# Performance work log

Hardware: AMD Instinct MI355X
Metric: run time of the kernel (lower is better)

## Reference

```python
import jax, jax.numpy as jnp
import numpy as np
from jax import lax

B, H, W = 2, 256, 256
K = 7
K2 = K * K
IN_CH = 32 * 2 + 81  # 145


def _conv(x, w, b):
    y = lax.conv_general_dilated(x, w, (1, 1), 'SAME', dimension_numbers=('NCHW', 'OIHW', 'NCHW'))
    return y + b[None, :, None, None]


def _lrelu(x):
    return jnp.where(x >= 0, x, 0.1 * x)


def _predictor(x, w1, b1, w2, b2, w3, b3, wo, bo, ww, bw):
    f = _lrelu(_conv(x, w1, b1))
    f = _lrelu(_conv(f, w2, b2))
    f = _lrelu(_conv(f, w3, b3))
    offsets = _conv(f, wo, bo)                     # (B, 2*K2, H, W)
    weights = jax.nn.softmax(_conv(f, ww, bw), 1)  # (B, K2, H, W)
    return offsets, weights


def _sample(image, offsets, weights):
    b, c, h, w = image.shape
    k2 = weights.shape[1]
    off = offsets.reshape(b, k2, 2, h, w)
    dx, dy = off[:, :, 0], off[:, :, 1]
    gy, gx = jnp.meshgrid(jnp.arange(h, dtype=image.dtype), jnp.arange(w, dtype=image.dtype), indexing='ij')
    sx = gx[None, None] + dx  # (b,k2,h,w)
    sy = gy[None, None] + dy
    # Original normalizes with 2*s/(n-1)-1 (align_corners=True formula) but calls
    # grid_sample(align_corners=False): pixel coord = ((g+1)*n - 1)/2 = s*n/(n-1) - 0.5.
    # padding_mode='border' == clamp coord to [0, n-1] before bilinear.
    px = jnp.clip(sx * (w / (w - 1.0)) - 0.5, 0.0, w - 1.0)
    py = jnp.clip(sy * (h / (h - 1.0)) - 0.5, 0.0, h - 1.0)
    x0 = jnp.floor(px)
    y0 = jnp.floor(py)
    fx = (px - x0)[:, None]  # (b,1,k2,h,w)
    fy = (py - y0)[:, None]
    x0i = x0.astype(jnp.int32)
    y0i = y0.astype(jnp.int32)
    x1i = jnp.minimum(x0i + 1, w - 1)
    y1i = jnp.minimum(y0i + 1, h - 1)
    img = image.reshape(b, c, h * w)

    def gather(yi, xi):
        idx = (yi * w + xi).reshape(b, 1, k2 * h * w)
        return jnp.take_along_axis(img, idx, axis=2).reshape(b, c, k2, h, w)

    v00 = gather(y0i, x0i)
    v01 = gather(y0i, x1i)
    v10 = gather(y1i, x0i)
    v11 = gather(y1i, x1i)
    sampled = (v00 * (1 - fx) * (1 - fy) + v01 * fx * (1 - fy)
               + v10 * (1 - fx) * fy + v11 * fx * fy)
    return jnp.einsum('bkhw,bckhw->bchw', weights, sampled)


def setup_inputs() -> dict:
    key = jax.random.key(0)
    ks = iter(jax.random.split(key, 64))

    def nrm(shape, s=1.0):
        return jax.random.normal(next(ks), shape, jnp.float32) * s

    off0 = np.array([[j - K // 2, i - K // 2] for i in range(K) for j in range(K)],
                    np.float32).reshape(-1)  # interleaved (dx, dy) default grid

    def pred_params(p):
        return {
            p + '_w1': nrm((256, IN_CH, 3, 3), 0.02), p + '_b1': jnp.zeros((256,), jnp.float32),
            p + '_w2': nrm((256, 256, 3, 3), 0.02), p + '_b2': jnp.zeros((256,), jnp.float32),
            p + '_w3': nrm((128, 256, 3, 3), 0.02), p + '_b3': jnp.zeros((128,), jnp.float32),
            p + '_wo': nrm((2 * K2, 128, 3, 3), 0.01), p + '_bo': jnp.asarray(off0),
            p + '_ww': nrm((K2, 128, 3, 3), 0.02), p + '_bw': jnp.full((K2,), 1.0 / K2, jnp.float32),
        }

    inp = {
        'frame1': nrm((B, 3, H, W)),
        'frame2': nrm((B, 3, H, W)),
        'feat1': nrm((B, 32, H, W)),
        'feat2': nrm((B, 32, H, W)),
        'corr': nrm((B, 81, H, W)),
    }
    inp.update(pred_params('k1'))
    inp.update(pred_params('k2'))
    inp['bl_w1'] = nrm((64, IN_CH, 3, 3), 0.02)
    inp['bl_b1'] = jnp.zeros((64,), jnp.float32)
    inp['bl_w2'] = nrm((1, 64, 3, 3), 0.02)
    inp['bl_b2'] = jnp.zeros((1,), jnp.float32)
    return inp


def reference(frame1, frame2, feat1, feat2, corr,
              k1_w1, k1_b1, k1_w2, k1_b2, k1_w3, k1_b3, k1_wo, k1_bo, k1_ww, k1_bw,
              k2_w1, k2_b1, k2_w2, k2_b2, k2_w3, k2_b3, k2_wo, k2_bo, k2_ww, k2_bw,
              bl_w1, bl_b1, bl_w2, bl_b2):
    combined = jnp.concatenate([feat1, feat2, corr], axis=1)  # (B,145,H,W)
    off1, wt1 = _predictor(combined, k1_w1, k1_b1, k1_w2, k1_b2, k1_w3, k1_b3, k1_wo, k1_bo, k1_ww, k1_bw)
    off2, wt2 = _predictor(combined, k2_w1, k2_b1, k2_w2, k2_b2, k2_w3, k2_b3, k2_wo, k2_bo, k2_ww, k2_bw)
    s1 = _sample(frame1, off1, wt1)
    s2 = _sample(frame2, off2, wt2)
    blend = jax.nn.sigmoid(_conv(_lrelu(_conv(combined, bl_w1, bl_b1)), bl_w2, bl_b2))
    output = blend * s1 + (1.0 - blend) * s2
    return (output, blend, off1, off2, wt1, wt2)
```

## Files before the change

### kernel.cpp

```cpp
#include <hip/hip_runtime.h>


static constexpr int HW  = 65536;
static constexpr int WID = 256;
static constexpr int PAD = 66564;

using f32x4  = __attribute__((ext_vector_type(4))) float;
using s16x8  = __attribute__((ext_vector_type(8))) short;

__device__ __forceinline__ unsigned short f2b(float f) {
    unsigned u = __builtin_bit_cast(unsigned, f);
    u += 0x7fffu + ((u >> 16) & 1u);
    return (unsigned short)(u >> 16);
}
__device__ __forceinline__ float b2f(unsigned short h) {
    unsigned u = ((unsigned)h) << 16;
    return __builtin_bit_cast(float, u);
}

template <int N> __device__ __forceinline__ void vm_wait() {
    asm volatile("s_waitcnt vmcnt(%0)" :: "n"(N) : "memory");
}

__global__ void pack_x(const float* __restrict__ feat1, const float* __restrict__ feat2,
                       const float* __restrict__ corr, unsigned short* __restrict__ Xc) {
    int idx = blockIdx.x * 256 + threadIdx.x;
    int g  = idx >> 17;
    int bp = idx & (2 * HW - 1);
    int b  = bp >> 16, p = bp & 65535;
    unsigned short v[8];
#pragma unroll
    for (int j = 0; j < 8; ++j) {
        int c = g * 8 + j;
        float val = 0.f;
        if (c < 32)       val = feat1[(size_t)(b * 32 + c) * HW + p];
        else if (c < 64)  val = feat2[(size_t)(b * 32 + (c - 32)) * HW + p];
        else if (c < 145) val = corr [(size_t)(b * 81 + (c - 64)) * HW + p];
        v[j] = f2b(val);
    }
    uint4 u;
    u.x = v[0] | ((unsigned)v[1] << 16);
    u.y = v[2] | ((unsigned)v[3] << 16);
    u.z = v[4] | ((unsigned)v[5] << 16);
    u.w = v[6] | ((unsigned)v[7] << 16);
    int y = p >> 8, x = p & 255;
    size_t cell = (size_t)b * PAD + (size_t)(y + 1) * 258 + (x + 1);
    *reinterpret_cast<uint4*>(Xc + cell * 160 + g * 8) = u;
}

__global__ void pack_w(const float* __restrict__ W, unsigned short* __restrict__ Wp,
                       int OC, int IC, int OCP, int KC) {
    int idx = blockIdx.x * 256 + threadIdx.x;
    int total = 9 * KC * 4 * OCP * 8;
    if (idx >= total) return;
    int i8 = idx & 7;  int r = idx >> 3;
    int oc = r % OCP;  r /= OCP;
    int g  = r & 3;    r >>= 2;
    int kb = r % KC;   int s = r / KC;
    int ic = kb * 32 + g * 8 + i8;
    float v = (oc < OC && ic < IC) ? W[((size_t)(oc * IC + ic)) * 9 + s] : 0.f;
    Wp[idx] = f2b(v);
}

__global__ void zero_border(unsigned short* __restrict__ buf, int C) {
    int idx = blockIdx.x * 256 + threadIdx.x;
    int G = C >> 3;
    int total = 2 * 1028 * G;
    if (idx >= total) return;
    int gi = idx % G; int r = idx / G;
    int ci = r % 1028; int b = r / 1028;
    int row, col;
    if (ci < 258)      { row = 0;            col = ci; }
    else if (ci < 516) { row = 257;          col = ci - 258; }
    else if (ci < 772) { row = ci - 516 + 1; col = 0; }
    else               { row = ci - 772 + 1; col = 257; }
    *reinterpret_cast<uint4*>(buf + ((size_t)b * PAD + row * 258 + col) * C + gi * 8) =
        make_uint4(0u, 0u, 0u, 0u);
}

template <int ICP, int OCF, int OCT, int MODE>
__global__ __launch_bounds__(512, 2) void conv3x3(
    const unsigned short* __restrict__ X,
    const uint4* __restrict__ Wp,
    const float* __restrict__ bias,
    unsigned short* __restrict__ outB,
    float* __restrict__ outF)
{
    constexpr int KC  = ICP / 32;
    constexpr int MF  = OCF / 32;
    constexpr int WST = OCF / 128;
    constexpr int WGR = OCF * 4;
    __shared__ uint4 lds[3072 + 3 * WGR];

    const int t = threadIdx.x;
    const int lane = t & 63;
    const int wv = t >> 6;
    const int wm = wv >> 2, wn = wv & 3;
    const int l15 = lane & 15, kq = lane >> 4;

    const int bid = blockIdx.x;
    const int work = ((bid & 7) << 6) | (bid >> 3);
    const int bb = work >> 8;
    const int tt = work & 255;
    const int tr = tt >> 3, tc = tt & 7;

    unsigned xoff[3];
#pragma unroll
    for (int it = 0; it < 3; ++it) {
        int G = it * 512 + t;
        int g = G / 384;
        int cell = G - g * 384;
        cell = min(cell, 339);
        int rr = cell / 34, cc = cell - rr * 34;
        xoff[it] = (unsigned)(((bb * PAD + (tr * 8 + rr) * 258 + tc * 32 + cc) * ICP
                               + g * 8) * 2);
    }
    const int tdst = t & ~63;

    auto gload = [&](const char* src, uint4* dst) {
        __builtin_amdgcn_global_load_lds(
            (const __attribute__((address_space(1))) unsigned int*)src,
            (__attribute__((address_space(3))) unsigned int*)dst, 16, 0, 0);
    };
    auto stage_x = [&](int slot) {
#pragma unroll
        for (int it = 0; it < 3; ++it)
            gload((const char*)X + xoff[it], &lds[slot * 1536 + it * 512 + tdst]);
    };
    auto stage_w = [&](int s2, int kb2, int slot) {
        const unsigned base = (unsigned)(s2 * KC + kb2) * (unsigned)(WGR * 16);
#pragma unroll
        for (int it = 0; it < WST; ++it)
            gload((const char*)Wp + base + (unsigned)((it * 512 + t) * 16),
                  &lds[3072 + slot * WGR + it * 512 + tdst]);
    };

    const unsigned aLane = (unsigned)((kq * OCF + wm * (OCF / 2) + l15) * 16) + 49152u;
    const unsigned bLane = (unsigned)((kq * 384 + wn * 68 + l15) * 16);
    const char* ldsc = (const char*)lds;

    f32x4 acc[MF][4] = {};

    stage_x(0);
    stage_w(0, 0, 0);
    stage_w(1, 0, 1);
    vm_wait<WST>();
    __builtin_amdgcn_s_barrier();

#pragma unroll 1
    for (int kb = 0; kb < KC; ++kb) {
        const unsigned bBase = bLane + (unsigned)((kb & 1) * 24576);
#pragma unroll
        for (int s = 0; s < 9; ++s) {
            const int dy = s / 3, dx = s - 3 * (s / 3);
            const unsigned aBase = aLane + (unsigned)((s % 3) * (WGR * 16));

            uint4 aR[MF], bR[4];
#pragma unroll
            for (int fm = 0; fm < MF; ++fm)
                aR[fm] = *(const uint4*)(ldsc + aBase + (unsigned)(fm * 256));
#pragma unroll
            for (int fn = 0; fn < 4; ++fn)
                bR[fn] = *(const uint4*)(ldsc + bBase +
                    (unsigned)(((((fn >> 1) + dy) * 34) + (fn & 1) * 16 + dx) * 16));

            if (s < 7) {
                stage_w(s + 2, kb, (s + 2) % 3);
            } else if (kb + 1 < KC) {
                stage_w(s - 7, kb + 1, (s + 2) % 3);
            }
            if (s == 0 && kb + 1 < KC) {
#pragma unroll
                for (int it = 0; it < 3; ++it) xoff[it] += 64u;
                stage_x((kb + 1) & 1);
            }

            __builtin_amdgcn_s_barrier();
            asm volatile("s_waitcnt lgkmcnt(0)" ::: "memory");
            __builtin_amdgcn_sched_barrier(0);
            __builtin_amdgcn_s_setprio(1);
#pragma unroll
            for (int fm = 0; fm < MF; ++fm)
#pragma unroll
                for (int fn = 0; fn < 4; ++fn)
                    acc[fm][fn] = __builtin_amdgcn_mfma_f32_16x16x32_bf16(
                        __builtin_bit_cast(s16x8, aR[fm]),
                        __builtin_bit_cast(s16x8, bR[fn]),
                        acc[fm][fn], 0, 0, 0);
            __builtin_amdgcn_s_setprio(0);

            if (s == 0) {
                if (kb + 1 < KC) vm_wait<WST + 3>(); else vm_wait<WST>();
            } else if (s < 7) {
                vm_wait<WST>();
            } else {
                if (kb + 1 < KC) vm_wait<WST>(); else vm_wait<0>();
            }
            __builtin_amdgcn_s_barrier();
        }
    }

#pragma unroll
    for (int fm = 0; fm < MF; ++fm) {
#pragma unroll
        for (int fn = 0; fn < 4; ++fn) {
            const int prow = wn * 2 + (fn >> 1);
            const int pcol = (fn & 1) * 16 + l15;
            const int oc0 = wm * (OCF / 2) + fm * 16 + kq * 4;
            if (MODE == 0) {
                if (oc0 < OCT) {
                    const size_t cellp = (size_t)bb * PAD +
                        (size_t)(tr * 8 + prow + 1) * 258 + tc * 32 + pcol + 1;
                    float4 bv = *reinterpret_cast<const float4*>(bias + oc0);
                    const float* bvp = reinterpret_cast<const float*>(&bv);
                    unsigned short o[4];
#pragma unroll
                    for (int j = 0; j < 4; ++j) {
                        float r = acc[fm][fn][j] + bvp[j];
                        r = (r >= 0.f) ? r : 0.1f * r;
                        o[j] = f2b(r);
                    }
                    uint2 pk;
                    pk.x = o[0] | ((unsigned)o[1] << 16);
                    pk.y = o[2] | ((unsigned)o[3] << 16);
                    *reinterpret_cast<uint2*>(outB + cellp * OCT + oc0) = pk;
                }
            } else {
                const int py = tr * 8 + prow, px = tc * 32 + pcol;
#pragma unroll
                for (int j = 0; j < 4; ++j) {
                    const int oc = oc0 + j;
                    if (oc < OCT)
                        outF[((size_t)bb * OCT + oc) * HW + py * WID + px] =
                            acc[fm][fn][j] + bias[oc];
                }
            }
        }
    }
}

__global__ void softmax49(float* __restrict__ L) {
    int idx = blockIdx.x * 256 + threadIdx.x;
    int b = idx >> 16, p = idx & 65535;
    float* lp = L + (size_t)b * 49 * HW + p;
    float v[49];
    float mx = -1e30f;
#pragma unroll
    for (int k = 0; k < 49; ++k) { v[k] = lp[(size_t)k * HW]; mx = fmaxf(mx, v[k]); }
    float sum = 0.f;
#pragma unroll
    for (int k = 0; k < 49; ++k) { v[k] = expf(v[k] - mx); sum += v[k]; }
    float inv = 1.f / sum;
#pragma unroll
    for (int k = 0; k < 49; ++k) lp[(size_t)k * HW] = v[k] * inv;
}

__global__ void blend2k(const unsigned short* __restrict__ Fb, const float* __restrict__ W2,
                        const float* __restrict__ B2, float* __restrict__ blendOut) {
    int idx = blockIdx.x * 256 + threadIdx.x;
    int b = idx >> 16, p = idx & 65535, y = p >> 8, x = p & 255;
    float acc = B2[0];
#pragma unroll
    for (int ry = 0; ry < 3; ++ry) {
#pragma unroll
        for (int rx = 0; rx < 3; ++rx) {
            const unsigned short* fp = Fb + ((size_t)b * PAD + (size_t)(y + ry) * 258 + (x + rx)) * 64;
#pragma unroll
            for (int g = 0; g < 8; ++g) {
                uint4 u = *reinterpret_cast<const uint4*>(fp + g * 8);
                unsigned w[4] = {u.x, u.y, u.z, u.w};
#pragma unroll
                for (int h = 0; h < 4; ++h) {
                    int c = g * 8 + h * 2;
                    acc += b2f((unsigned short)(w[h] & 0xffffu)) * W2[(c)     * 9 + ry * 3 + rx];
                    acc += b2f((unsigned short)(w[h] >> 16))     * W2[(c + 1) * 9 + ry * 3 + rx];
                }
            }
        }
    }
    blendOut[idx] = 1.f / (1.f + expf(-acc));
}

__global__ void pack_frames(const float* __restrict__ f1, const float* __restrict__ f2,
                            f32x4* __restrict__ Ff) {
    int idx = blockIdx.x * 256 + threadIdx.x;
    int fr = idx >> 17; int bp = idx & (2 * HW - 1);
    const float* src = fr ? f2 : f1;
    int b = bp >> 16, p = bp & 65535;
    f32x4 v;
    v[0] = src[(size_t)(b * 3 + 0) * HW + p];
    v[1] = src[(size_t)(b * 3 + 1) * HW + p];
    v[2] = src[(size_t)(b * 3 + 2) * HW + p];
    v[3] = 0.f;
    Ff[(size_t)fr * 2 * HW + bp] = v;
}

__device__ __forceinline__ void sample_accum4(const f32x4* __restrict__ img,
                                              const float* __restrict__ off,
                                              const float* __restrict__ wt,
                                              int x, int y, f32x4& s) {
    for (int k = 0; k < 49; ++k) {
        float dx = off[(size_t)(2 * k) * HW];
        float dy = off[(size_t)(2 * k + 1) * HW];
        float w  = wt [(size_t)k * HW];
        float px = ((float)x + dx) * (256.f / 255.f) - 0.5f;
        float py = ((float)y + dy) * (256.f / 255.f) - 0.5f;
        px = fminf(fmaxf(px, 0.f), 255.f);
        py = fminf(fmaxf(py, 0.f), 255.f);
        float x0f = floorf(px), y0f = floorf(py);
        float fx = px - x0f, fy = py - y0f;
        int x0 = (int)x0f, y0 = (int)y0f;
        int x1 = min(x0 + 1, 255), y1 = min(y0 + 1, 255);
        const f32x4* r0 = img + y0 * WID;
        const f32x4* r1 = img + y1 * WID;
        f32x4 v = (1.f - fy) * ((1.f - fx) * r0[x0] + fx * r0[x1]) +
                  fy         * ((1.f - fx) * r1[x0] + fx * r1[x1]);
        s += w * v;
    }
}

__global__ void sample_final(const f32x4* __restrict__ Ff,
                             const float* __restrict__ off1, const float* __restrict__ off2,
                             const float* __restrict__ wt1, const float* __restrict__ wt2,
                             const float* __restrict__ blend, float* __restrict__ out) {
    int idx = blockIdx.x * 256 + threadIdx.x;
    int b = idx >> 16, p = idx & 65535, y = p >> 8, x = p & 255;
    f32x4 s1 = {0.f, 0.f, 0.f, 0.f}, s2 = {0.f, 0.f, 0.f, 0.f};
    sample_accum4(Ff + (size_t)b * HW, off1 + (size_t)b * 98 * HW + p,
                  wt1 + (size_t)b * 49 * HW + p, x, y, s1);
    sample_accum4(Ff + (size_t)(2 + b) * HW, off2 + (size_t)b * 98 * HW + p,
                  wt2 + (size_t)b * 49 * HW + p, x, y, s2);
    float bl = blend[idx];
#pragma unroll
    for (int c = 0; c < 3; ++c)
        out[(size_t)(b * 3 + c) * HW + p] = bl * s1[c] + (1.f - bl) * s2[c];
}

extern "C" void kernel_launch(void* const* d_in, const int* in_sizes, int n_in,
                              void* d_out, int out_size, void* d_ws, size_t ws_size,
                              hipStream_t stream) {
    (void)in_sizes; (void)n_in; (void)out_size; (void)ws_size;
    const float* frame1 = (const float*)d_in[0];
    const float* frame2 = (const float*)d_in[1];
    const float* feat1  = (const float*)d_in[2];
    const float* feat2  = (const float*)d_in[3];
    const float* corr   = (const float*)d_in[4];
    const float* Wsrc[2][5];
    const float* Bsrc[2][5];
    for (int pdx = 0; pdx < 2; ++pdx) {
        int base = 5 + pdx * 10;
        for (int l = 0; l < 5; ++l) {
            Wsrc[pdx][l] = (const float*)d_in[base + 2 * l];
            Bsrc[pdx][l] = (const float*)d_in[base + 2 * l + 1];
        }
    }
    const float* bl_w1 = (const float*)d_in[25];
    const float* bl_b1 = (const float*)d_in[26];
    const float* bl_w2 = (const float*)d_in[27];
    const float* bl_b2 = (const float*)d_in[28];

    float* out      = (float*)d_out;
    float* out_bl   = out + 393216;
    float* out_off[2] = {out + 524288,   out + 13369344};
    float* out_wt [2] = {out + 26214400, out + 32636928};

    char* ws = (char*)d_ws;
    size_t o = 0;
    auto alloc = [&](size_t bytes) { char* p = ws + o; o += (bytes + 255) & ~(size_t)255; return p; };
    unsigned short* Xc   = (unsigned short*)alloc((size_t)2 * PAD * 160 * 2);
    unsigned short* bufA = (unsigned short*)alloc((size_t)2 * PAD * 256 * 2);
    unsigned short* bufB = (unsigned short*)alloc((size_t)2 * PAD * 256 * 2);
    unsigned short *WpC1[2], *WpC2[2], *WpC3[2], *WpCo[2], *WpCw[2];
    for (int pdx = 0; pdx < 2; ++pdx) {
        WpC1[pdx] = (unsigned short*)alloc((size_t)9 * 256 * 160 * 2);
        WpC2[pdx] = (unsigned short*)alloc((size_t)9 * 256 * 256 * 2);
        WpC3[pdx] = (unsigned short*)alloc((size_t)9 * 128 * 256 * 2);
        WpCo[pdx] = (unsigned short*)alloc((size_t)9 * 128 * 128 * 2);
        WpCw[pdx] = (unsigned short*)alloc((size_t)9 * 128 * 128 * 2);
    }
    unsigned short* WpBl = (unsigned short*)alloc((size_t)9 * 128 * 160 * 2);
    f32x4* Ff = (f32x4*)bufA;

    auto packw = [&](const float* W, unsigned short* Wp, int OC, int IC, int OCP, int ICP) {
        int total = 9 * OCP * ICP;
        pack_w<<<(total + 255) / 256, 256, 0, stream>>>(W, Wp, OC, IC, OCP, ICP / 32);
    };
    auto zb = [&](unsigned short* buf, int C) {
        int total = 2 * 1028 * (C / 8);
        zero_border<<<(total + 255) / 256, 256, 0, stream>>>(buf, C);
    };

    zb(Xc, 160);
    pack_x<<<(2 * HW * 20) / 256, 256, 0, stream>>>(feat1, feat2, corr, Xc);
    for (int pdx = 0; pdx < 2; ++pdx) {
        packw(Wsrc[pdx][0], WpC1[pdx], 256, 145, 256, 160);
        packw(Wsrc[pdx][1], WpC2[pdx], 256, 256, 256, 256);
        packw(Wsrc[pdx][2], WpC3[pdx], 128, 256, 128, 256);
        packw(Wsrc[pdx][3], WpCo[pdx],  98, 128, 128, 128);
        packw(Wsrc[pdx][4], WpCw[pdx],  49, 128, 128, 128);
    }
    packw(bl_w1, WpBl, 64, 145, 128, 160);
    zb(bufB, 256);

    for (int pdx = 0; pdx < 2; ++pdx) {
        zb(bufA, 256);
        conv3x3<160, 256, 256, 0><<<512, 512, 0, stream>>>(
            Xc, (const uint4*)WpC1[pdx], Bsrc[pdx][0], bufA, nullptr);
        conv3x3<256, 256, 256, 0><<<512, 512, 0, stream>>>(
            bufA, (const uint4*)WpC2[pdx], Bsrc[pdx][1], bufB, nullptr);
        zb(bufA, 128);
        conv3x3<256, 128, 128, 0><<<512, 512, 0, stream>>>(
            bufB, (const uint4*)WpC3[pdx], Bsrc[pdx][2], bufA, nullptr);
        conv3x3<128, 128, 98, 1><<<512, 512, 0, stream>>>(
            bufA, (const uint4*)WpCo[pdx], Bsrc[pdx][3], nullptr, out_off[pdx]);
        conv3x3<128, 128, 49, 1><<<512, 512, 0, stream>>>(
            bufA, (const uint4*)WpCw[pdx], Bsrc[pdx][4], nullptr, out_wt[pdx]);
        softmax49<<<512, 256, 0, stream>>>(out_wt[pdx]);
    }

    zb(bufB, 64);
    conv3x3<160, 128, 64, 0><<<512, 512, 0, stream>>>(
        Xc, (const uint4*)WpBl, bl_b1, bufB, nullptr);
    blend2k<<<512, 256, 0, stream>>>(bufB, bl_w2, bl_b2, out_bl);

    pack_frames<<<(4 * HW) / 256, 256, 0, stream>>>(frame1, frame2, Ff);
    sample_final<<<512, 256, 0, stream>>>(Ff, out_off[0], out_off[1],
                                          out_wt[0], out_wt[1], out_bl, out);
}
```

Baseline: 1.230 ms.

## Split conv output channels across grid, deepen weight pipeline, double-buffer LDS fragments

The conv3x3 kernel now always computes a 128-wide output-channel tile and splits wider layers across blockIdx.y, which halves the accumulator registers and raises the launch bound to 4 blocks per CU. Weight staging moves from 3 to 4 LDS slots. Fragment loads from LDS are double-buffered in registers, so the next tap's A/B operands are read while the current MFMAs run, and one barrier per step is dropped. The input tile for 256-channel layers is now loaded twice, once per channel half, and the added register buffers and occupancy target could raise spill risk.

Result: slower. 4.517 ms (+267.2%).

```diff
diff --git a/kernel.cpp b/kernel.cpp
--- a/kernel.cpp
+++ b/kernel.cpp
@@ -78,25 +78,23 @@
         make_uint4(0u, 0u, 0u, 0u);
 }
 
-template <int ICP, int OCF, int OCT, int MODE>
-__global__ __launch_bounds__(512, 2) void conv3x3(
+template <int ICP, int OCT, int MODE>
+__global__ __launch_bounds__(512, 4) void conv3x3(
     const unsigned short* __restrict__ X,
-    const uint4* __restrict__ Wp,
+    const uint4* __restrict__ Wp, int OCP,
     const float* __restrict__ bias,
     unsigned short* __restrict__ outB,
     float* __restrict__ outF)
 {
-    constexpr int KC  = ICP / 32;
-    constexpr int MF  = OCF / 32;
-    constexpr int WST = OCF / 128;
-    constexpr int WGR = OCF * 4;
-    __shared__ uint4 lds[3072 + 3 * WGR];
+    constexpr int KC = ICP / 32;
+    __shared__ uint4 lds[5120];
 
     const int t = threadIdx.x;
     const int lane = t & 63;
     const int wv = t >> 6;
     const int wm = wv >> 2, wn = wv & 3;
     const int l15 = lane & 15, kq = lane >> 4;
+    const int ocOff = blockIdx.y * 128;
 
     const int bid = blockIdx.x;
     const int work = ((bid & 7) << 6) | (bid >> 3);
@@ -128,85 +126,97 @@
             gload((const char*)X + xoff[it], &lds[slot * 1536 + it * 512 + tdst]);
     };
     auto stage_w = [&](int s2, int kb2, int slot) {
-        const unsigned base = (unsigned)(s2 * KC + kb2) * (unsigned)(WGR * 16);
-#pragma unroll
-        for (int it = 0; it < WST; ++it)
-            gload((const char*)Wp + base + (unsigned)((it * 512 + t) * 16),
-                  &lds[3072 + slot * WGR + it * 512 + tdst]);
+        const uint4* src = Wp + (size_t)((s2 * KC + kb2) * 4 + (t >> 7)) * OCP
+                              + ocOff + (t & 127);
+        gload((const char*)src, &lds[3072 + slot * 512 + tdst]);
     };
 
-    const unsigned aLane = (unsigned)((kq * OCF + wm * (OCF / 2) + l15) * 16) + 49152u;
+    const unsigned aLane = (unsigned)((kq * 128 + wm * 64 + l15) * 16);
     const unsigned bLane = (unsigned)((kq * 384 + wn * 68 + l15) * 16);
     const char* ldsc = (const char*)lds;
 
-    f32x4 acc[MF][4] = {};
+    f32x4 acc[4][4] = {};
+    uint4 aS[2][4], bS[2][4];
 
     stage_x(0);
     stage_w(0, 0, 0);
     stage_w(1, 0, 1);
-    vm_wait<WST>();
+    stage_w(2, 0, 2);
+    vm_wait<1>();
     __builtin_amdgcn_s_barrier();
+#pragma unroll
+    for (int fm = 0; fm < 4; ++fm)
+        aS[0][fm] = *(const uint4*)(ldsc + 49152u + aLane + (unsigned)(fm * 256));
+#pragma unroll
+    for (int fn = 0; fn < 4; ++fn)
+        bS[0][fn] = *(const uint4*)(ldsc + bLane +
+            (unsigned)((((fn >> 1) * 34) + (fn & 1) * 16) * 16));
+
+#define PH(S, CUR, NXT)                                                        \
+    {                                                                          \
+        if ((S) < 6) {                                                         \
+            stage_w((S) + 3, kb, (kb + (S) + 3) & 3);                          \
+        } else if (kb + 1 < KC) {                                              \
+            stage_w((S) - 6, kb + 1, (kb + (S) + 3) & 3);                      \
+        }                                                                      \
+        if ((S) == 0 && kb + 1 < KC) {                                         \
+            _Pragma("unroll")                                                  \
+            for (int it = 0; it < 3; ++it) xoff[it] += 64u;                    \
+            stage_x((kb + 1) & 1);                                             \
+        }                                                                      \
+        if ((S) == 0)      { if (kb + 1 < KC) vm_wait<4>(); else vm_wait<1>(); } \
+        else if ((S) < 6)  { vm_wait<1>(); }                                   \
+        else               { if (kb + 1 < KC) vm_wait<1>(); else vm_wait<0>(); } \
+        __builtin_amdgcn_s_setprio(1);                                         \
+        _Pragma("unroll")                                                      \
+        for (int fm = 0; fm < 4; ++fm)                                         \
+            _Pragma("unroll")                                                  \
+            for (int fn = 0; fn < 4; ++fn)                                     \
+                acc[fm][fn] = __builtin_amdgcn_mfma_f32_16x16x32_bf16(         \
+                    __builtin_bit_cast(s16x8, aS[CUR][fm]),                    \
+                    __builtin_bit_cast(s16x8, bS[CUR][fn]),                    \
+                    acc[fm][fn], 0, 0, 0);                                     \
+        __builtin_amdgcn_s_setprio(0);                                         \
+        if (!((S) == 8 && kb + 1 >= KC)) {                                     \
+            const int sN  = ((S) < 8) ? (S) + 1 : 0;                           \
+            const int dyN = sN / 3, dxN = sN - 3 * (sN / 3);                   \
+            const unsigned wbase = 49152u +                                    \
+                (unsigned)(((kb + (S) + 1) & 3) * 8192);                       \
+            const unsigned xb2 = ((S) == 8)                                    \
+                ? (unsigned)(((kb + 1) & 1) * 24576)                           \
+                : (unsigned)((kb & 1) * 24576);                                \
+            _Pragma("unroll")                                                  \
+            for (int fm = 0; fm < 4; ++fm)                                     \
+                aS[NXT][fm] = *(const uint4*)(ldsc + wbase + aLane +           \
+                                              (unsigned)(fm * 256));           \
+            _Pragma("unroll")                                                  \
+            for (int fn = 0; fn < 4; ++fn)                                     \
+                bS[NXT][fn] = *(const uint4*)(ldsc + xb2 + bLane +             \
+                    (unsigned)(((((fn >> 1) + dyN) * 34) +                     \
+                                (fn & 1) * 16 + dxN) * 16));                   \
+        }                                                                      \
+        __builtin_amdgcn_s_barrier();                                          \
+    }
 
 #pragma unroll 1
     for (int kb = 0; kb < KC; ++kb) {
-        const unsigned bBase = bLane + (unsigned)((kb & 1) * 24576);
-#pragma unroll
-        for (int s = 0; s < 9; ++s) {
-            const int dy = s / 3, dx = s - 3 * (s / 3);
-            const unsigned aBase = aLane + (unsigned)((s % 3) * (WGR * 16));
-
-            uint4 aR[MF], bR[4];
-#pragma unroll
-            for (int fm = 0; fm < MF; ++fm)
-                aR[fm] = *(const uint4*)(ldsc + aBase + (unsigned)(fm * 256));
-#pragma unroll
-            for (int fn = 0; fn < 4; ++fn)
-                bR[fn] = *(const uint4*)(ldsc + bBase +
-                    (unsigned)(((((fn >> 1) + dy) * 34) + (fn & 1) * 16 + dx) * 16));
-
-            if (s < 7) {
-                stage_w(s + 2, kb, (s + 2) % 3);
-            } else if (kb + 1 < KC) {
-                stage_w(s - 7, kb + 1, (s + 2) % 3);
-            }
-            if (s == 0 && kb + 1 < KC) {
-#pragma unroll
-                for (int it = 0; it < 3; ++it) xoff[it] += 64u;
-                stage_x((kb + 1) & 1);
-            }
-
-            __builtin_amdgcn_s_barrier();
-            asm volatile("s_waitcnt lgkmcnt(0)" ::: "memory");
-            __builtin_amdgcn_sched_barrier(0);
-            __builtin_amdgcn_s_setprio(1);
-#pragma unroll
-            for (int fm = 0; fm < MF; ++fm)
-#pragma unroll
-                for (int fn = 0; fn < 4; ++fn)
-                    acc[fm][fn] = __builtin_amdgcn_mfma_f32_16x16x32_bf16(
-                        __builtin_bit_cast(s16x8, aR[fm]),
-                        __builtin_bit_cast(s16x8, bR[fn]),
-                        acc[fm][fn], 0, 0, 0);
-            __builtin_amdgcn_s_setprio(0);
-
-            if (s == 0) {
-                if (kb + 1 < KC) vm_wait<WST + 3>(); else vm_wait<WST>();
-            } else if (s < 7) {
-                vm_wait<WST>();
-            } else {
-                if (kb + 1 < KC) vm_wait<WST>(); else vm_wait<0>();
-            }
-            __builtin_amdgcn_s_barrier();
+        if (!(kb & 1)) {
+            PH(0,0,1) PH(1,1,0) PH(2,0,1) PH(3,1,0) PH(4,0,1)
+            PH(5,1,0) PH(6,0,1) PH(7,1,0) PH(8,0,1)
+        } else {
+            PH(0,1,0) PH(1,0,1) PH(2,1,0) PH(3,0,1) PH(4,1,0)
+            PH(5,0,1) PH(6,1,0) PH(7,0,1) PH(8,1,0)
         }
     }
-
-#pragma unroll
-    for (int fm = 0; fm < MF; ++fm) {
+#undef PH
+
+#pragma unroll
+    for (int fm = 0; fm < 4; ++fm) {
 #pragma unroll
         for (int fn = 0; fn < 4; ++fn) {
             const int prow = wn * 2 + (fn >> 1);
             const int pcol = (fn & 1) * 16 + l15;
-            const int oc0 = wm * (OCF / 2) + fm * 16 + kq * 4;
+            const int oc0 = ocOff + wm * 64 + fm * 16 + kq * 4;
             if (MODE == 0) {
                 if (oc0 < OCT) {
                     const size_t cellp = (size_t)bb * PAD +
@@ -404,23 +414,23 @@
 
     for (int pdx = 0; pdx < 2; ++pdx) {
         zb(bufA, 256);
-        conv3x3<160, 256, 256, 0><<<512, 512, 0, stream>>>(
-            Xc, (const uint4*)WpC1[pdx], Bsrc[pdx][0], bufA, nullptr);
-        conv3x3<256, 256, 256, 0><<<512, 512, 0, stream>>>(
-            bufA, (const uint4*)WpC2[pdx], Bsrc[pdx][1], bufB, nullptr);
+        conv3x3<160, 256, 0><<<dim3(512, 2), 512, 0, stream>>>(
+            Xc, (const uint4*)WpC1[pdx], 256, Bsrc[pdx][0], bufA, nullptr);
+        conv3x3<256, 256, 0><<<dim3(512, 2), 512, 0, stream>>>(
+            bufA, (const uint4*)WpC2[pdx], 256, Bsrc[pdx][1], bufB, nullptr);
         zb(bufA, 128);
-        conv3x3<256, 128, 128, 0><<<512, 512, 0, stream>>>(
-            bufB, (const uint4*)WpC3[pdx], Bsrc[pdx][2], bufA, nullptr);
-        conv3x3<128, 128, 98, 1><<<512, 512, 0, stream>>>(
-            bufA, (const uint4*)WpCo[pdx], Bsrc[pdx][3], nullptr, out_off[pdx]);
-        conv3x3<128, 128, 49, 1><<<512, 512, 0, stream>>>(
-            bufA, (const uint4*)WpCw[pdx], Bsrc[pdx][4], nullptr, out_wt[pdx]);
+        conv3x3<256, 128, 0><<<dim3(512, 1), 512, 0, stream>>>(
+            bufB, (const uint4*)WpC3[pdx], 128, Bsrc[pdx][2], bufA, nullptr);
+        conv3x3<128, 98, 1><<<dim3(512, 1), 512, 0, stream>>>(
+            bufA, (const uint4*)WpCo[pdx], 128, Bsrc[pdx][3], nullptr, out_off[pdx]);
+        conv3x3<128, 49, 1><<<dim3(512, 1), 512, 0, stream>>>(
+            bufA, (const uint4*)WpCw[pdx], 128, Bsrc[pdx][4], nullptr, out_wt[pdx]);
         softmax49<<<512, 256, 0, stream>>>(out_wt[pdx]);
     }
 
     zb(bufB, 64);
-    conv3x3<160, 128, 64, 0><<<512, 512, 0, stream>>>(
-        Xc, (const uint4*)WpBl, bl_b1, bufB, nullptr);
+    conv3x3<160, 64, 0><<<dim3(512, 1), 512, 0, stream>>>(
+        Xc, (const uint4*)WpBl, 128, bl_b1, bufB, nullptr);
     blend2k<<<512, 256, 0, stream>>>(bufB, bl_w2, bl_b2, out_bl);
 
     pack_frames<<<(4 * HW) / 256, 256, 0, stream>>>(frame1, frame2, Ff);
```
